# Kernel optimization log

Hardware: AMD Instinct MI355X
Metric: run time of the kernel (lower is better)

## Reference

```python
import jax, jax.numpy as jnp
import numpy as np

B, T, E = 2, 2048, 1024
H = 16
D = E // H  # head_dim = 64


def setup_inputs() -> dict:
    key = jax.random.key(0)
    ks = jax.random.split(key, 9)
    s = 1.0 / np.sqrt(E)
    inp = {"x": jax.random.normal(ks[0], (B, T, E), dtype=jnp.float32)}
    # Linear params (torch nn.Linear: y = x @ W.T + b)
    inp["Wq"] = jax.random.uniform(ks[1], (E, E), jnp.float32, -s, s)
    inp["bq"] = jax.random.uniform(ks[2], (E,), jnp.float32, -s, s)
    inp["Wk"] = jax.random.uniform(ks[3], (E, E), jnp.float32, -s, s)
    inp["bk"] = jax.random.uniform(ks[4], (E,), jnp.float32, -s, s)
    inp["Wv"] = jax.random.uniform(ks[5], (E, E), jnp.float32, -s, s)
    inp["bv"] = jax.random.uniform(ks[6], (E,), jnp.float32, -s, s)
    inp["Wo"] = jax.random.uniform(ks[7], (E, E), jnp.float32, -s, s)
    inp["bo"] = jax.random.uniform(ks[8], (E,), jnp.float32, -s, s)
    return inp


def reference(x, Wq, bq, Wk, bk, Wv, bv, Wo, bo):
    # QKV projections, reshape to [B, H, T, D]
    def split_heads(y):
        return y.reshape(B, T, H, D).transpose(0, 2, 1, 3)

    Q = split_heads(x @ Wq.T + bq)
    K = split_heads(x @ Wk.T + bk)
    V = split_heads(x @ Wv.T + bv)

    scale = 1.0 / jnp.sqrt(jnp.asarray(D, x.dtype))
    scores = jnp.einsum("bhqd,bhkd->bhqk", Q, K) * scale  # [B,H,T,T]
    attn = jax.nn.softmax(scores, axis=-1)
    out = jnp.einsum("bhqk,bhkd->bhqd", attn, V)  # [B,H,T,D]
    out = out.transpose(0, 2, 1, 3).reshape(B, T, E)
    # dropout is identity in eval mode
    return out @ Wo.T + bo
```

## Files before the change

### kernel.cpp

```cpp
#include <hip/hip_runtime.h>
#include <math.h>

#define BB 2
#define TT 2048
#define EE 1024
#define HH 16
#define DD 64
#define MM (BB*TT)
#define KK EE

typedef short bf16x8 __attribute__((ext_vector_type(8)));
typedef float f32x4  __attribute__((ext_vector_type(4)));

__device__ __forceinline__ unsigned short f2bf(float f) {
  unsigned int u = __float_as_uint(f);
  u = (u + 0x7FFFu + ((u >> 16) & 1u)) >> 16;
  return (unsigned short)u;
}

__device__ __forceinline__ void async16(const void* g, void* l) {
  __builtin_amdgcn_global_load_lds(
      (const __attribute__((address_space(1))) unsigned int*)g,
      (__attribute__((address_space(3))) unsigned int*)l, 16, 0, 0);
}

__global__ __launch_bounds__(256) void to_bf16(
    const float* __restrict__ x,  const float* __restrict__ wq,
    const float* __restrict__ wk, const float* __restrict__ wv,
    const float* __restrict__ wo,
    unsigned short* __restrict__ xh, unsigned short* __restrict__ wcat,
    unsigned short* __restrict__ woh)
{
  int c = blockIdx.x * 256 + threadIdx.x;
  const float* src; unsigned short* dst; int off;
  if (c < 1048576) { src = x; dst = xh; off = c; }
  else {
    int r = c - 1048576;
    int w = r >> 18;
    off = r & 262143;
    if      (w == 0) { src = wq; dst = wcat; }
    else if (w == 1) { src = wk; dst = wcat + (1 << 20); }
    else if (w == 2) { src = wv; dst = wcat + (2 << 20); }
    else             { src = wo; dst = woh; }
  }
  float4 v = ((const float4*)src)[off];
  ushort4 h;
  h.x = f2bf(v.x); h.y = f2bf(v.y); h.z = f2bf(v.z); h.w = f2bf(v.w);
  ((ushort4*)dst)[off] = h;
}

template<int MODE>
__global__ __launch_bounds__(256) void gemm_bf16(
    const unsigned short* __restrict__ A, const unsigned short* __restrict__ B,
    const float* __restrict__ b0p, const float* __restrict__ b1p,
    const float* __restrict__ b2p,
    unsigned short* __restrict__ oq, unsigned short* __restrict__ ok,
    unsigned short* __restrict__ ov, float* __restrict__ ofp, float qscale)
{
  constexpr int NT = (MODE == 0) ? 128 : 64;
  constexpr int JN = NT / 32;
  constexpr int BROWS = NT * 32;
  __shared__ unsigned short S[(MODE == 0) ? 17408 : 12288];

  const int tid  = threadIdx.x;
  const int lane = tid & 63;
  const int wv   = tid >> 6;
  const int col  = lane & 15;
  const int quad = lane >> 4;
  const int wm = (wv >> 1) * 64;
  const int wn = (wv & 1) * (NT / 2);
  const int m0 = blockIdx.x * 128;
  const int n0 = blockIdx.y * NT;

  const int srow = lane >> 2;
  const int sw16 = (((lane & 3) ^ ((lane >> 2) & 3)) << 3);
  const int fswA = ((quad ^ (col & 3)) << 3);

  constexpr int NW = (MODE == 0) ? 4 : 3;
  auto stage = [&](int kt, int b) {
#pragma unroll
    for (int s = 0; s < NW; ++s) {
      const int t = wv * NW + s;
      const unsigned short* src; int rb, g0, loff;
      if (t < 8) { src = A; rb = t * 16;       g0 = m0; loff = b * 4096; }
      else       { src = B; rb = (t - 8) * 16; g0 = n0; loff = 8192 + b * BROWS; }
      async16(src + (size_t)(g0 + rb + srow) * KK + kt + sw16,
              S + loff + rb * 32);
    }
  };

  f32x4 acc[4][JN];
  const f32x4 z = {0.f, 0.f, 0.f, 0.f};
#pragma unroll
  for (int i = 0; i < 4; ++i)
#pragma unroll
    for (int j = 0; j < JN; ++j) acc[i][j] = z;

  stage(0, 0);
  __syncthreads();

  for (int kt = 0; kt < KK; kt += 32) {
    const int buf = (kt >> 5) & 1;
    if (kt + 32 < KK) stage(kt + 32, buf ^ 1);

    const unsigned short* Asb = S + buf * 4096;
    const unsigned short* Bsb = S + 8192 + buf * BROWS;
    bf16x8 bf[JN];
#pragma unroll
    for (int j = 0; j < JN; ++j)
      bf[j] = *(const bf16x8*)(Bsb + (wn + j * 16 + col) * 32 + fswA);
#pragma unroll
    for (int i = 0; i < 4; ++i) {
      bf16x8 af = *(const bf16x8*)(Asb + (wm + i * 16 + col) * 32 + fswA);
#pragma unroll
      for (int j = 0; j < JN; ++j)
        acc[i][j] = __builtin_amdgcn_mfma_f32_16x16x32_bf16(af, bf[j], acc[i][j], 0, 0, 0);
    }
    __syncthreads();
  }

  unsigned short* Cs = S;
  if (MODE == 0) {
    const int region = n0 >> 10;
    const float* bias = (region == 0) ? b0p : (region == 1) ? b1p : b2p;
    const float scl = (region == 0) ? qscale : 1.0f;
    const int nlbase = n0 & 1023;
    const int h0 = nlbase >> 6;
    const int b = m0 >> 11, t0 = m0 & (TT - 1);
    if (region < 2) {
#pragma unroll
      for (int i = 0; i < 4; ++i)
#pragma unroll
        for (int j = 0; j < 4; ++j) {
          const int nt = wn + j * 16 + col;
          const float bs = bias[nlbase + nt];
#pragma unroll
          for (int r = 0; r < 4; ++r) {
            const int mt = wm + i * 16 + quad * 4 + r;
            Cs[mt * 136 + nt] = f2bf((acc[i][j][r] + bs) * scl);
          }
        }
      __syncthreads();
      unsigned short* dst = (region == 0) ? oq : ok;
#pragma unroll
      for (int s = 0; s < 8; ++s) {
        const int u = s * 256 + tid;
        const int mt = u >> 4, hs = (u >> 3) & 1, ch = u & 7;
        const size_t g = ((size_t)(b * HH + h0 + hs) * TT + t0 + mt) * DD + ch * 8;
        *(uint4*)(dst + g) = *(const uint4*)(Cs + mt * 136 + hs * 64 + ch * 8);
      }
    } else {
#pragma unroll
      for (int i = 0; i < 4; ++i)
#pragma unroll
        for (int j = 0; j < 4; ++j) {
          const int nt = wn + j * 16 + col;
          const float bs = bias[nlbase + nt];
          ushort4 pk;
          pk.x = f2bf(acc[i][j][0] + bs);
          pk.y = f2bf(acc[i][j][1] + bs);
          pk.z = f2bf(acc[i][j][2] + bs);
          pk.w = f2bf(acc[i][j][3] + bs);
          *(ushort4*)(Cs + nt * 136 + wm + i * 16 + quad * 4) = pk;
        }
      __syncthreads();
#pragma unroll
      for (int s = 0; s < 8; ++s) {
        const int u = s * 256 + tid;
        const int nt = u >> 4, ch = u & 15;
        const int d = nt & 63, hs = nt >> 6;
        const size_t g = ((size_t)(b * HH + h0 + hs) * DD + d) * TT + t0 + ch * 8;
        *(uint4*)(ov + g) = *(const uint4*)(Cs + nt * 136 + ch * 8);
      }
    }
  } else {
#pragma unroll
    for (int i = 0; i < 4; ++i) {
#pragma unroll
      for (int j = 0; j < JN; ++j) {
        const int n = n0 + wn + j * 16 + col;
        const float bs = b0p[n];
#pragma unroll
        for (int r = 0; r < 4; ++r) {
          const int m = m0 + wm + i * 16 + quad * 4 + r;
          ofp[(size_t)m * EE + n] = acc[i][j][r] + bs;
        }
      }
    }
  }
}

__global__ __launch_bounds__(256) void flash_mfma(
    const unsigned short* __restrict__ Qb, const unsigned short* __restrict__ Kb,
    const unsigned short* __restrict__ Vtb, unsigned short* __restrict__ ctx)
{
  __shared__ unsigned short QPs[128 * 72];
  __shared__ unsigned short Ks[2][64 * 64];
  __shared__ unsigned short Vts[2][64 * 64];

  const int tid  = threadIdx.x;
  const int lane = tid & 63;
  const int wv   = tid >> 6;
  const int col  = lane & 15;
  const int quad = lane >> 4;
  const int wm   = wv * 32;
  const int q0   = blockIdx.x * 128;
  const int bh   = blockIdx.y;

  const unsigned short* Qg = Qb  + (size_t)bh * TT * DD;
  const unsigned short* Kg = Kb  + (size_t)bh * TT * DD;
  const unsigned short* Vg = Vtb + (size_t)bh * DD * TT;

  const int srow = lane >> 3;
  const int sw16 = (((lane & 7) ^ ((lane >> 3) & 7)) << 3);
  const int cxor = (col & 7);

  auto stage_kv = [&](int kt, int b) {
#pragma unroll
    for (int s = 0; s < 4; ++s) {
      const int rb = (wv & 1) * 32 + s * 8;
      if (wv < 2)
        async16(Kg + (size_t)(kt + rb + srow) * DD + sw16, &Ks[b][rb * 64]);
      else
        async16(Vg + (size_t)(rb + srow) * TT + kt + sw16, &Vts[b][rb * 64]);
    }
  };

#pragma unroll
  for (int s = 0; s < 4; ++s) {
    const int rb = wv * 32 + s * 8;
    async16(Qg + (size_t)(q0 + rb + srow) * DD + sw16, &QPs[rb * 64]);
  }
  stage_kv(0, 0);
  __syncthreads();

  bf16x8 aq[2][2];
#pragma unroll
  for (int i = 0; i < 2; ++i)
#pragma unroll
    for (int h = 0; h < 2; ++h)
      aq[i][h] = *(const bf16x8*)(QPs + (wm + i * 16 + col) * 64 +
                                  (((h * 4 + quad) ^ cxor) << 3));
  __syncthreads();

  f32x4 o_acc[2][4];
  float lpart[2];
  const f32x4 z = {0.f, 0.f, 0.f, 0.f};
#pragma unroll
  for (int i = 0; i < 2; ++i) {
    lpart[i] = 0.f;
#pragma unroll
    for (int j = 0; j < 4; ++j) o_acc[i][j] = z;
  }

  for (int kt = 0; kt < TT; kt += 64) {
    const int buf = (kt >> 6) & 1;
    if (kt + 64 < TT) stage_kv(kt + 64, buf ^ 1);

    f32x4 sacc[2][4];
#pragma unroll
    for (int i = 0; i < 2; ++i)
#pragma unroll
      for (int j = 0; j < 4; ++j) sacc[i][j] = z;

#pragma unroll
    for (int j = 0; j < 4; ++j) {
      bf16x8 bk0 = *(const bf16x8*)(Ks[buf] + (j * 16 + col) * 64 + ((quad ^ cxor) << 3));
      bf16x8 bk1 = *(const bf16x8*)(Ks[buf] + (j * 16 + col) * 64 + (((4 + quad) ^ cxor) << 3));
#pragma unroll
      for (int i = 0; i < 2; ++i) {
        sacc[i][j] = __builtin_amdgcn_mfma_f32_16x16x32_bf16(bk0, aq[i][0], sacc[i][j], 0, 0, 0);
        sacc[i][j] = __builtin_amdgcn_mfma_f32_16x16x32_bf16(bk1, aq[i][1], sacc[i][j], 0, 0, 0);
      }
    }

#pragma unroll
    for (int i = 0; i < 2; ++i) {
      const int prow = (wm + i * 16 + col) * 72;
      float lp = 0.f;
#pragma unroll
      for (int j = 0; j < 4; ++j) {
        float p0 = __builtin_amdgcn_exp2f(sacc[i][j][0]);
        float p1 = __builtin_amdgcn_exp2f(sacc[i][j][1]);
        float p2 = __builtin_amdgcn_exp2f(sacc[i][j][2]);
        float p3 = __builtin_amdgcn_exp2f(sacc[i][j][3]);
        lp += (p0 + p1) + (p2 + p3);
        uint2 w;
        w.x = __builtin_amdgcn_perm(__float_as_uint(p1), __float_as_uint(p0), 0x07060302u);
        w.y = __builtin_amdgcn_perm(__float_as_uint(p3), __float_as_uint(p2), 0x07060302u);
        *(uint2*)(QPs + prow + j * 16 + quad * 4) = w;
      }
      lpart[i] += lp;
    }

    bf16x8 ap[2][2];
#pragma unroll
    for (int i = 0; i < 2; ++i) {
      ap[i][0] = *(const bf16x8*)(QPs + (wm + i * 16 + col) * 72 + quad * 8);
      ap[i][1] = *(const bf16x8*)(QPs + (wm + i * 16 + col) * 72 + 32 + quad * 8);
    }

#pragma unroll
    for (int j = 0; j < 4; ++j) {
      bf16x8 bv0 = *(const bf16x8*)(Vts[buf] + (j * 16 + col) * 64 + ((quad ^ cxor) << 3));
      bf16x8 bv1 = *(const bf16x8*)(Vts[buf] + (j * 16 + col) * 64 + (((4 + quad) ^ cxor) << 3));
#pragma unroll
      for (int i = 0; i < 2; ++i) {
        o_acc[i][j] = __builtin_amdgcn_mfma_f32_16x16x32_bf16(ap[i][0], bv0, o_acc[i][j], 0, 0, 0);
        o_acc[i][j] = __builtin_amdgcn_mfma_f32_16x16x32_bf16(ap[i][1], bv1, o_acc[i][j], 0, 0, 0);
      }
    }

    __syncthreads();
  }

  unsigned short* Cs = &Ks[0][0];
  const int b = bh >> 4, h = bh & 15;
#pragma unroll
  for (int i = 0; i < 2; ++i) {
    float l = lpart[i];
    l += __shfl_xor(l, 16);
    l += __shfl_xor(l, 32);
#pragma unroll
    for (int r = 0; r < 4; ++r) {
      const float inv = 1.0f / __shfl(l, quad * 4 + r);
      const int trow = wm + i * 16 + quad * 4 + r;
#pragma unroll
      for (int j = 0; j < 4; ++j) {
        const int n = j * 16 + col;
        const int ch = ((n >> 3) ^ (trow & 7)) << 3;
        Cs[trow * 64 + ch + (n & 7)] = f2bf(o_acc[i][j][r] * inv);
      }
    }
  }
  __syncthreads();
#pragma unroll
  for (int s = 0; s < 4; ++s) {
    const int u = s * 256 + tid;
    const int mr = u >> 3, ch = u & 7;
    const size_t g = ((size_t)(b * TT + q0 + mr)) * EE + h * DD + ch * 8;
    const int chs = (ch ^ (mr & 7)) << 3;
    *(uint4*)(ctx + g) = *(const uint4*)(Cs + mr * 64 + chs);
  }
}

extern "C" void kernel_launch(void* const* d_in, const int* in_sizes, int n_in,
                              void* d_out, int out_size, void* d_ws, size_t ws_size,
                              hipStream_t stream) {
  const float* x  = (const float*)d_in[0];
  const float* Wq = (const float*)d_in[1];
  const float* bq = (const float*)d_in[2];
  const float* Wk = (const float*)d_in[3];
  const float* bk = (const float*)d_in[4];
  const float* Wv = (const float*)d_in[5];
  const float* bv = (const float*)d_in[6];
  const float* Wo = (const float*)d_in[7];
  const float* bo = (const float*)d_in[8];

  unsigned short* p = (unsigned short*)d_ws;
  const size_t XN = (size_t)MM * EE;
  const size_t WN = (size_t)EE * EE;
  unsigned short* x_h    = p;           p += XN;
  unsigned short* Wcat_h = p;           p += 3 * WN;
  unsigned short* Wo_h   = p;           p += WN;
  unsigned short* Qb     = p;           p += XN;
  unsigned short* Kb     = p;           p += XN;
  unsigned short* Vtb    = p;           p += XN;
  unsigned short* ctx_h  = x_h;

  to_bf16<<<8192, 256, 0, stream>>>(x, Wq, Wk, Wv, Wo, x_h, Wcat_h, Wo_h);

  const float qscale = 0.125f * 1.44269504088896f;

  gemm_bf16<0><<<dim3(MM / 128, 3 * EE / 128), 256, 0, stream>>>(
      x_h, Wcat_h, bq, bk, bv, Qb, Kb, Vtb, nullptr, qscale);

  flash_mfma<<<dim3(TT / 128, BB * HH), 256, 0, stream>>>(Qb, Kb, Vtb, ctx_h);

  gemm_bf16<2><<<dim3(MM / 128, EE / 64), 256, 0, stream>>>(
      ctx_h, Wo_h, bo, nullptr, nullptr,
      nullptr, nullptr, nullptr, (float*)d_out, 1.0f);
}
```

Measured before the change: 212.6 us.

## Use 512-thread blocks with finer per-wave tiles in GEMM and flash kernels

```diff
diff --git a/kernel.cpp b/kernel.cpp
--- a/kernel.cpp
+++ b/kernel.cpp
@@ -50,7 +50,7 @@
 }
 
 template<int MODE>
-__global__ __launch_bounds__(256) void gemm_bf16(
+__global__ __launch_bounds__(512) void gemm_bf16(
     const unsigned short* __restrict__ A, const unsigned short* __restrict__ B,
     const float* __restrict__ b0p, const float* __restrict__ b1p,
     const float* __restrict__ b2p,
@@ -60,6 +60,7 @@
   constexpr int NT = (MODE == 0) ? 128 : 64;
   constexpr int JN = NT / 32;
   constexpr int BROWS = NT * 32;
+  constexpr int TOT = (MODE == 0) ? 16 : 12;
   __shared__ unsigned short S[(MODE == 0) ? 17408 : 12288];
 
   const int tid  = threadIdx.x;
@@ -67,8 +68,8 @@
   const int wv   = tid >> 6;
   const int col  = lane & 15;
   const int quad = lane >> 4;
-  const int wm = (wv >> 1) * 64;
-  const int wn = (wv & 1) * (NT / 2);
+  const int wm = (wv & 3) * 32;
+  const int wn = (wv >> 2) * (NT / 2);
   const int m0 = blockIdx.x * 128;
   const int n0 = blockIdx.y * NT;
 
@@ -76,23 +77,24 @@
   const int sw16 = (((lane & 3) ^ ((lane >> 2) & 3)) << 3);
   const int fswA = ((quad ^ (col & 3)) << 3);
 
-  constexpr int NW = (MODE == 0) ? 4 : 3;
   auto stage = [&](int kt, int b) {
 #pragma unroll
-    for (int s = 0; s < NW; ++s) {
-      const int t = wv * NW + s;
-      const unsigned short* src; int rb, g0, loff;
-      if (t < 8) { src = A; rb = t * 16;       g0 = m0; loff = b * 4096; }
-      else       { src = B; rb = (t - 8) * 16; g0 = n0; loff = 8192 + b * BROWS; }
-      async16(src + (size_t)(g0 + rb + srow) * KK + kt + sw16,
-              S + loff + rb * 32);
+    for (int s = 0; s < 2; ++s) {
+      const int t = wv * 2 + s;
+      if (t < TOT) {
+        const unsigned short* src; int rb, g0, loff;
+        if (t < 8) { src = A; rb = t * 16;       g0 = m0; loff = b * 4096; }
+        else       { src = B; rb = (t - 8) * 16; g0 = n0; loff = 8192 + b * BROWS; }
+        async16(src + (size_t)(g0 + rb + srow) * KK + kt + sw16,
+                S + loff + rb * 32);
+      }
     }
   };
 
-  f32x4 acc[4][JN];
+  f32x4 acc[2][JN];
   const f32x4 z = {0.f, 0.f, 0.f, 0.f};
 #pragma unroll
-  for (int i = 0; i < 4; ++i)
+  for (int i = 0; i < 2; ++i)
 #pragma unroll
     for (int j = 0; j < JN; ++j) acc[i][j] = z;
 
@@ -110,7 +112,7 @@
     for (int j = 0; j < JN; ++j)
       bf[j] = *(const bf16x8*)(Bsb + (wn + j * 16 + col) * 32 + fswA);
 #pragma unroll
-    for (int i = 0; i < 4; ++i) {
+    for (int i = 0; i < 2; ++i) {
       bf16x8 af = *(const bf16x8*)(Asb + (wm + i * 16 + col) * 32 + fswA);
 #pragma unroll
       for (int j = 0; j < JN; ++j)
@@ -129,7 +131,7 @@
     const int b = m0 >> 11, t0 = m0 & (TT - 1);
     if (region < 2) {
 #pragma unroll
-      for (int i = 0; i < 4; ++i)
+      for (int i = 0; i < 2; ++i)
 #pragma unroll
         for (int j = 0; j < 4; ++j) {
           const int nt = wn + j * 16 + col;
@@ -143,15 +145,15 @@
       __syncthreads();
       unsigned short* dst = (region == 0) ? oq : ok;
 #pragma unroll
-      for (int s = 0; s < 8; ++s) {
-        const int u = s * 256 + tid;
+      for (int s = 0; s < 4; ++s) {
+        const int u = s * 512 + tid;
         const int mt = u >> 4, hs = (u >> 3) & 1, ch = u & 7;
         const size_t g = ((size_t)(b * HH + h0 + hs) * TT + t0 + mt) * DD + ch * 8;
         *(uint4*)(dst + g) = *(const uint4*)(Cs + mt * 136 + hs * 64 + ch * 8);
       }
     } else {
 #pragma unroll
-      for (int i = 0; i < 4; ++i)
+      for (int i = 0; i < 2; ++i)
 #pragma unroll
         for (int j = 0; j < 4; ++j) {
           const int nt = wn + j * 16 + col;
@@ -165,8 +167,8 @@
         }
       __syncthreads();
 #pragma unroll
-      for (int s = 0; s < 8; ++s) {
-        const int u = s * 256 + tid;
+      for (int s = 0; s < 4; ++s) {
+        const int u = s * 512 + tid;
         const int nt = u >> 4, ch = u & 15;
         const int d = nt & 63, hs = nt >> 6;
         const size_t g = ((size_t)(b * HH + h0 + hs) * DD + d) * TT + t0 + ch * 8;
@@ -175,7 +177,7 @@
     }
   } else {
 #pragma unroll
-    for (int i = 0; i < 4; ++i) {
+    for (int i = 0; i < 2; ++i) {
 #pragma unroll
       for (int j = 0; j < JN; ++j) {
         const int n = n0 + wn + j * 16 + col;
@@ -190,7 +192,7 @@
   }
 }
 
-__global__ __launch_bounds__(256) void flash_mfma(
+__global__ __launch_bounds__(512) void flash_mfma(
     const unsigned short* __restrict__ Qb, const unsigned short* __restrict__ Kb,
     const unsigned short* __restrict__ Vtb, unsigned short* __restrict__ ctx)
 {
@@ -203,9 +205,10 @@
   const int wv   = tid >> 6;
   const int col  = lane & 15;
   const int quad = lane >> 4;
-  const int wm   = wv * 32;
-  const int q0   = blockIdx.x * 128;
-  const int bh   = blockIdx.y;
+  const int wm   = wv * 16;
+  const int gid  = blockIdx.x;
+  const int bh   = gid & 31;
+  const int q0   = (gid >> 5) * 128;
 
   const unsigned short* Qg = Qb  + (size_t)bh * TT * DD;
   const unsigned short* Kg = Kb  + (size_t)bh * TT * DD;
@@ -217,9 +220,9 @@
 
   auto stage_kv = [&](int kt, int b) {
 #pragma unroll
-    for (int s = 0; s < 4; ++s) {
-      const int rb = (wv & 1) * 32 + s * 8;
-      if (wv < 2)
+    for (int s = 0; s < 2; ++s) {
+      const int rb = (wv & 3) * 16 + s * 8;
+      if (wv < 4)
         async16(Kg + (size_t)(kt + rb + srow) * DD + sw16, &Ks[b][rb * 64]);
       else
         async16(Vg + (size_t)(rb + srow) * TT + kt + sw16, &Vts[b][rb * 64]);
@@ -227,88 +230,69 @@
   };
 
 #pragma unroll
-  for (int s = 0; s < 4; ++s) {
-    const int rb = wv * 32 + s * 8;
+  for (int s = 0; s < 2; ++s) {
+    const int rb = wv * 16 + s * 8;
     async16(Qg + (size_t)(q0 + rb + srow) * DD + sw16, &QPs[rb * 64]);
   }
   stage_kv(0, 0);
   __syncthreads();
 
-  bf16x8 aq[2][2];
-#pragma unroll
-  for (int i = 0; i < 2; ++i)
-#pragma unroll
-    for (int h = 0; h < 2; ++h)
-      aq[i][h] = *(const bf16x8*)(QPs + (wm + i * 16 + col) * 64 +
-                                  (((h * 4 + quad) ^ cxor) << 3));
+  bf16x8 aq[2];
+#pragma unroll
+  for (int h = 0; h < 2; ++h)
+    aq[h] = *(const bf16x8*)(QPs + (wm + col) * 64 +
+                             (((h * 4 + quad) ^ cxor) << 3));
   __syncthreads();
 
-  f32x4 o_acc[2][4];
-  float lpart[2];
+  f32x4 o_acc[4];
+  float lpart = 0.f;
   const f32x4 z = {0.f, 0.f, 0.f, 0.f};
 #pragma unroll
-  for (int i = 0; i < 2; ++i) {
-    lpart[i] = 0.f;
-#pragma unroll
-    for (int j = 0; j < 4; ++j) o_acc[i][j] = z;
-  }
+  for (int j = 0; j < 4; ++j) o_acc[j] = z;
 
   for (int kt = 0; kt < TT; kt += 64) {
     const int buf = (kt >> 6) & 1;
     if (kt + 64 < TT) stage_kv(kt + 64, buf ^ 1);
 
-    f32x4 sacc[2][4];
-#pragma unroll
-    for (int i = 0; i < 2; ++i)
-#pragma unroll
-      for (int j = 0; j < 4; ++j) sacc[i][j] = z;
+    f32x4 sacc[4];
+#pragma unroll
+    for (int j = 0; j < 4; ++j) sacc[j] = z;
 
 #pragma unroll
     for (int j = 0; j < 4; ++j) {
       bf16x8 bk0 = *(const bf16x8*)(Ks[buf] + (j * 16 + col) * 64 + ((quad ^ cxor) << 3));
       bf16x8 bk1 = *(const bf16x8*)(Ks[buf] + (j * 16 + col) * 64 + (((4 + quad) ^ cxor) << 3));
-#pragma unroll
-      for (int i = 0; i < 2; ++i) {
-        sacc[i][j] = __builtin_amdgcn_mfma_f32_16x16x32_bf16(bk0, aq[i][0], sacc[i][j], 0, 0, 0);
-        sacc[i][j] = __builtin_amdgcn_mfma_f32_16x16x32_bf16(bk1, aq[i][1], sacc[i][j], 0, 0, 0);
-      }
-    }
-
-#pragma unroll
-    for (int i = 0; i < 2; ++i) {
-      const int prow = (wm + i * 16 + col) * 72;
+      sacc[j] = __builtin_amdgcn_mfma_f32_16x16x32_bf16(bk0, aq[0], sacc[j], 0, 0, 0);
+      sacc[j] = __builtin_amdgcn_mfma_f32_16x16x32_bf16(bk1, aq[1], sacc[j], 0, 0, 0);
+    }
+
+    {
+      const int prow = (wm + col) * 72;
       float lp = 0.f;
 #pragma unroll
       for (int j = 0; j < 4; ++j) {
-        float p0 = __builtin_amdgcn_exp2f(sacc[i][j][0]);
-        float p1 = __builtin_amdgcn_exp2f(sacc[i][j][1]);
-        float p2 = __builtin_amdgcn_exp2f(sacc[i][j][2]);
-        float p3 = __builtin_amdgcn_exp2f(sacc[i][j][3]);
+        float p0 = __builtin_amdgcn_exp2f(sacc[j][0]);
+        float p1 = __builtin_amdgcn_exp2f(sacc[j][1]);
+        float p2 = __builtin_amdgcn_exp2f(sacc[j][2]);
+        float p3 = __builtin_amdgcn_exp2f(sacc[j][3]);
         lp += (p0 + p1) + (p2 + p3);
         uint2 w;
         w.x = __builtin_amdgcn_perm(__float_as_uint(p1), __float_as_uint(p0), 0x07060302u);
         w.y = __builtin_amdgcn_perm(__float_as_uint(p3), __float_as_uint(p2), 0x07060302u);
         *(uint2*)(QPs + prow + j * 16 + quad * 4) = w;
       }
-      lpart[i] += lp;
-    }
-
-    bf16x8 ap[2][2];
-#pragma unroll
-    for (int i = 0; i < 2; ++i) {
-      ap[i][0] = *(const bf16x8*)(QPs + (wm + i * 16 + col) * 72 + quad * 8);
-      ap[i][1] = *(const bf16x8*)(QPs + (wm + i * 16 + col) * 72 + 32 + quad * 8);
-    }
+      lpart += lp;
+    }
+
+    bf16x8 ap0 = *(const bf16x8*)(QPs + (wm + col) * 72 + quad * 8);
+    bf16x8 ap1 = *(const bf16x8*)(QPs + (wm + col) * 72 + 32 + quad * 8);
 
 #pragma unroll
     for (int j = 0; j < 4; ++j) {
       bf16x8 bv0 = *(const bf16x8*)(Vts[buf] + (j * 16 + col) * 64 + ((quad ^ cxor) << 3));
       bf16x8 bv1 = *(const bf16x8*)(Vts[buf] + (j * 16 + col) * 64 + (((4 + quad) ^ cxor) << 3));
-#pragma unroll
-      for (int i = 0; i < 2; ++i) {
-        o_acc[i][j] = __builtin_amdgcn_mfma_f32_16x16x32_bf16(ap[i][0], bv0, o_acc[i][j], 0, 0, 0);
-        o_acc[i][j] = __builtin_amdgcn_mfma_f32_16x16x32_bf16(ap[i][1], bv1, o_acc[i][j], 0, 0, 0);
-      }
+      o_acc[j] = __builtin_amdgcn_mfma_f32_16x16x32_bf16(ap0, bv0, o_acc[j], 0, 0, 0);
+      o_acc[j] = __builtin_amdgcn_mfma_f32_16x16x32_bf16(ap1, bv1, o_acc[j], 0, 0, 0);
     }
 
     __syncthreads();
@@ -316,27 +300,24 @@
 
   unsigned short* Cs = &Ks[0][0];
   const int b = bh >> 4, h = bh & 15;
-#pragma unroll
-  for (int i = 0; i < 2; ++i) {
-    float l = lpart[i];
-    l += __shfl_xor(l, 16);
-    l += __shfl_xor(l, 32);
-#pragma unroll
-    for (int r = 0; r < 4; ++r) {
-      const float inv = 1.0f / __shfl(l, quad * 4 + r);
-      const int trow = wm + i * 16 + quad * 4 + r;
-#pragma unroll
-      for (int j = 0; j < 4; ++j) {
-        const int n = j * 16 + col;
-        const int ch = ((n >> 3) ^ (trow & 7)) << 3;
-        Cs[trow * 64 + ch + (n & 7)] = f2bf(o_acc[i][j][r] * inv);
-      }
+  float l = lpart;
+  l += __shfl_xor(l, 16);
+  l += __shfl_xor(l, 32);
+#pragma unroll
+  for (int r = 0; r < 4; ++r) {
+    const float inv = 1.0f / __shfl(l, quad * 4 + r);
+    const int trow = wm + quad * 4 + r;
+#pragma unroll
+    for (int j = 0; j < 4; ++j) {
+      const int n = j * 16 + col;
+      const int ch = ((n >> 3) ^ (trow & 7)) << 3;
+      Cs[trow * 64 + ch + (n & 7)] = f2bf(o_acc[j][r] * inv);
     }
   }
   __syncthreads();
 #pragma unroll
-  for (int s = 0; s < 4; ++s) {
-    const int u = s * 256 + tid;
+  for (int s = 0; s < 2; ++s) {
+    const int u = s * 512 + tid;
     const int mr = u >> 3, ch = u & 7;
     const size_t g = ((size_t)(b * TT + q0 + mr)) * EE + h * DD + ch * 8;
     const int chs = (ch ^ (mr & 7)) << 3;
@@ -372,12 +353,12 @@
 
   const float qscale = 0.125f * 1.44269504088896f;
 
-  gemm_bf16<0><<<dim3(MM / 128, 3 * EE / 128), 256, 0, stream>>>(
+  gemm_bf16<0><<<dim3(MM / 128, 3 * EE / 128), 512, 0, stream>>>(
       x_h, Wcat_h, bq, bk, bv, Qb, Kb, Vtb, nullptr, qscale);
 
-  flash_mfma<<<dim3(TT / 128, BB * HH), 256, 0, stream>>>(Qb, Kb, Vtb, ctx_h);
-
-  gemm_bf16<2><<<dim3(MM / 128, EE / 64), 256, 0, stream>>>(
+  flash_mfma<<<dim3((TT / 128) * BB * HH), 512, 0, stream>>>(Qb, Kb, Vtb, ctx_h);
+
+  gemm_bf16<2><<<dim3(MM / 128, EE / 64), 512, 0, stream>>>(
       ctx_h, Wo_h, bo, nullptr, nullptr,
       nullptr, nullptr, nullptr, (float*)d_out, 1.0f);
 }
```

After: 193.3 us. 9.1% less time.
